# Kernel optimization log

Measured on AMD Instinct MI355X. Metric: run time of the kernel, lower is better.

Reference implementation:

```python
import jax, jax.numpy as jnp
import numpy as np

N = 100000      # nodes
E = 1600000     # edges (avg degree 16)
DIN = 32
DOUT = 32


def setup_inputs() -> dict:
    key = jax.random.key(0)
    k1, k2, k3 = jax.random.split(key, 3)
    x = jax.random.normal(k1, (N, DIN), dtype=jnp.float32)
    edge_index = jax.random.randint(k2, (2, E), 0, N)  # [2, E] (src, dst)
    W = jax.random.normal(k3, (DIN, DOUT), dtype=jnp.float32) / np.sqrt(DIN).astype(np.float32)
    b = jnp.zeros((DOUT,), dtype=jnp.float32)
    return {"x": x, "edge_index": edge_index, "W": W, "b": b}


def reference(x, edge_index, W, b):
    # GCNConv with norm='both' (DGL GraphConv semantics):
    # out = D_dst^{-1/2} * A * (D_src^{-1/2} * X * W) + b
    src, dst = edge_index[0], edge_index[1]
    ones = jnp.ones((edge_index.shape[1],), dtype=x.dtype)
    out_deg = jax.ops.segment_sum(ones, src, num_segments=N)  # out-degree of src nodes
    in_deg = jax.ops.segment_sum(ones, dst, num_segments=N)   # in-degree of dst nodes
    norm_src = jnp.where(out_deg > 0, out_deg ** -0.5, 0.0)   # [N]
    norm_dst = jnp.where(in_deg > 0, in_deg ** -0.5, 0.0)     # [N]
    # feature transform before aggregation (in_feats >= out_feats path)
    h = (x * norm_src[:, None]) @ W                           # [N, DOUT]
    # sparse neighbor aggregation: gather along src, scatter-add to dst
    agg = jax.ops.segment_sum(h[src], dst, num_segments=N)    # [N, DOUT]
    return agg * norm_dst[:, None] + b
```

## Files before the change

### kernel.cpp

```cpp
#include <hip/hip_runtime.h>
#include <hip/hip_bf16.h>

#define DIN 32
#define DOUT 32
#define BINSHIFT 8
#define BINW 256
#define NBMAX 512
#define PTHREADS 512
#define PK 8
#define PB (PTHREADS * PK)
#define SRCBITS 17
#define SRCMASK ((1u << SRCBITS) - 1u)
#define CAP_LDS 8192

__device__ __forceinline__ float bf_lo(unsigned v) { return __uint_as_float(v << 16); }
__device__ __forceinline__ float bf_hi(unsigned v) { return __uint_as_float(v & 0xffff0000u); }
__device__ __forceinline__ unsigned f2bf_rne(float f) {
    unsigned u = __float_as_uint(f);
    return (u + 0x7fffu + ((u >> 16) & 1u)) >> 16;
}

__global__ void init_caps_kernel(int* __restrict__ baseS, int* __restrict__ baseD,
                                 int* __restrict__ curS, int* __restrict__ curD,
                                 int NB, int cap) {
    int i = threadIdx.x;
    if (i <= NB) {
        int v = i * cap;
        baseS[i] = v; baseD[i] = v;
        if (i < NB) { curS[i] = v; curD[i] = v; }
    }
}

__global__ void hist_coarse_kernel(const int* __restrict__ src, const int* __restrict__ dst,
                                   int E, int* __restrict__ gcntS, int* __restrict__ gcntD) {
    __shared__ int hS[NBMAX], hD[NBMAX];
    for (int i = threadIdx.x; i < NBMAX; i += 256) { hS[i] = 0; hD[i] = 0; }
    __syncthreads();
    int stride = gridDim.x * blockDim.x;
    for (int e = blockIdx.x * blockDim.x + threadIdx.x; e < E; e += stride) {
        atomicAdd(&hS[src[e] >> BINSHIFT], 1);
        atomicAdd(&hD[dst[e] >> BINSHIFT], 1);
    }
    __syncthreads();
    for (int i = threadIdx.x; i < NBMAX; i += 256) {
        if (hS[i]) atomicAdd(&gcntS[i], hS[i]);
        if (hD[i]) atomicAdd(&gcntD[i], hD[i]);
    }
}

__global__ void scan_coarse_kernel(const int* __restrict__ gcntS, const int* __restrict__ gcntD,
                                   int* __restrict__ baseS, int* __restrict__ baseD,
                                   int* __restrict__ curS, int* __restrict__ curD,
                                   int NB, int E) {
    __shared__ int s1[NBMAX], s2[NBMAX];
    int t = threadIdx.x;
    int a = (t < NB) ? gcntS[t] : 0;
    int c = (t < NB) ? gcntD[t] : 0;
    s1[t] = a; s2[t] = c;
    for (int o = 1; o < NBMAX; o <<= 1) {
        __syncthreads();
        int x = (t >= o) ? s1[t - o] : 0;
        int y = (t >= o) ? s2[t - o] : 0;
        __syncthreads();
        s1[t] += x; s2[t] += y;
    }
    __syncthreads();
    if (t < NB) {
        baseS[t] = s1[t] - a; curS[t] = s1[t] - a;
        baseD[t] = s2[t] - c; curD[t] = s2[t] - c;
    }
    if (t == 0) { baseS[NB] = E; baseD[NB] = E; }
}

__global__ void partition_both_kernel(const int* __restrict__ src, const int* __restrict__ dst,
                                      int E, int* __restrict__ curS, int* __restrict__ curD,
                                      int* __restrict__ binnedS, int* __restrict__ binnedD) {
    __shared__ int cntS[NBMAX], cntD[NBMAX];
    __shared__ int gbS[NBMAX], gbD[NBMAX];
    __shared__ int stage[PB];
    __shared__ unsigned short sbin[PB];
    int t = threadIdx.x;
    cntS[t] = 0; cntD[t] = 0;
    __syncthreads();

    int base_e = blockIdx.x * PB;
    int nvalid = E - base_e; if (nvalid > PB) nvalid = PB;

    int vs[PK], vd[PK], rkS[PK], rkD[PK];
#pragma unroll
    for (int i = 0; i < PK; ++i) {
        int e = base_e + i * PTHREADS + t;
        if (e < E) {
            int s = src[e], d = dst[e];
            vs[i] = s; vd[i] = d;
            rkS[i] = atomicAdd(&cntS[s >> BINSHIFT], 1);
            rkD[i] = atomicAdd(&cntD[d >> BINSHIFT], 1);
        } else vs[i] = -1;
    }
    __syncthreads();

    int cS = cntS[t], cD = cntD[t];
    for (int o = 1; o < NBMAX; o <<= 1) {
        __syncthreads();
        int xS = (t >= o) ? cntS[t - o] : 0;
        int xD = (t >= o) ? cntD[t - o] : 0;
        __syncthreads();
        cntS[t] += xS; cntD[t] += xD;
    }
    __syncthreads();
    int lS = cntS[t] - cS, lD = cntD[t] - cD;
    int gS = cS ? atomicAdd(&curS[t], cS) : 0;
    int gD = cD ? atomicAdd(&curD[t], cD) : 0;
    gbS[t] = gS - lS; gbD[t] = gD - lD;
    __syncthreads();
    cntS[t] = lS; cntD[t] = lD;
    __syncthreads();

#pragma unroll
    for (int i = 0; i < PK; ++i) {
        if (vs[i] >= 0) {
            int b = vs[i] >> BINSHIFT;
            int slot = cntS[b] + rkS[i];
            stage[slot] = vs[i];
            sbin[slot] = (unsigned short)b;
        }
    }
    __syncthreads();
    for (int i = t; i < nvalid; i += PTHREADS)
        binnedS[gbS[sbin[i]] + i] = stage[i];
    __syncthreads();

#pragma unroll
    for (int i = 0; i < PK; ++i) {
        if (vs[i] >= 0) {
            int b = vd[i] >> BINSHIFT;
            int slot = cntD[b] + rkD[i];
            stage[slot] = ((vd[i] & (BINW - 1)) << SRCBITS) | vs[i];
            sbin[slot] = (unsigned short)b;
        }
    }
    __syncthreads();
    for (int i = t; i < nvalid; i += PTHREADS)
        binnedD[gbD[sbin[i]] + i] = stage[i];
}

__global__ void count_src_kernel(const int* __restrict__ binnedS, const int* __restrict__ baseS,
                                 const int* __restrict__ endS, int* __restrict__ degs, int n) {
    __shared__ int cnt[BINW];
    int b = blockIdx.x;
    int beg = baseS[b], end = endS[b];
    int lo = b << BINSHIFT;
    int t = threadIdx.x;
    cnt[t] = 0;
    __syncthreads();
    for (int e = beg + t; e < end; e += 256) atomicAdd(&cnt[binnedS[e] - lo], 1);
    __syncthreads();
    int node = lo + t;
    if (node < n) degs[node] = cnt[t];
}

__global__ void transform_bf16_kernel(const float* __restrict__ x, const float* __restrict__ W,
                                      const int* __restrict__ degs,
                                      unsigned* __restrict__ h, int n) {
    __shared__ float Ws[32][33];
    __shared__ float xs[16][32];
    int pr = threadIdx.x & 15;
    int r  = threadIdx.x >> 4;

    for (int i = threadIdx.x; i < 32 * 32; i += 256) Ws[i >> 5][i & 31] = W[i];
    int row = blockIdx.x * 16 + r;
    if (row < n) {
        float2 xv = *reinterpret_cast<const float2*>(&x[(size_t)row * 32 + 2 * pr]);
        xs[r][2 * pr] = xv.x; xs[r][2 * pr + 1] = xv.y;
    }
    __syncthreads();

    if (row < n) {
        float a0 = 0.f, a1 = 0.f;
#pragma unroll
        for (int k = 0; k < 32; ++k) {
            float xv = xs[r][k];
            a0 += xv * Ws[k][2 * pr];
            a1 += xv * Ws[k][2 * pr + 1];
        }
        int d = degs[row];
        float nrm = (d > 0) ? rsqrtf((float)d) : 0.f;
        h[(size_t)row * 16 + pr] = f2bf_rne(a0 * nrm) | (f2bf_rne(a1 * nrm) << 16);
    }
}

__global__ void csr_agg_kernel(const int* __restrict__ binnedD, const int* __restrict__ baseD,
                               const int* __restrict__ endD, const uint2* __restrict__ hb,
                               const float* __restrict__ bias, float* __restrict__ out, int n) {
    __shared__ int cnt[BINW];
    __shared__ int start[BINW];
    __shared__ int cur[BINW];
    __shared__ int lesrc[CAP_LDS];

    int t = threadIdx.x;
    int b = blockIdx.x;
    int beg = baseD[b], end = endD[b];
    int lo = b << BINSHIFT;
    int q  = t & 7;
    int ng = t >> 3;

    float4 a0 = {0.f, 0.f, 0.f, 0.f};
    float4 a1 = {0.f, 0.f, 0.f, 0.f};
    int d0 = 0, d1 = 0;

    for (int cb = beg; cb < end; cb += CAP_LDS) {
        int ce = cb + CAP_LDS; if (ce > end) ce = end;
        if (t < BINW) cnt[t] = 0;
        __syncthreads();
        for (int e = cb + t; e < ce; e += 1024)
            atomicAdd(&cnt[((unsigned)binnedD[e]) >> SRCBITS], 1);
        __syncthreads();
        if (t < BINW) start[t] = cnt[t];
        __syncthreads();
        for (int o = 1; o < BINW; o <<= 1) {
            int x = 0;
            if (t < BINW && t >= o) x = start[t - o];
            __syncthreads();
            if (t < BINW) start[t] += x;
            __syncthreads();
        }
        if (t < BINW) { int excl = start[t] - cnt[t]; start[t] = excl; cur[t] = excl; }
        __syncthreads();
        for (int e = cb + t; e < ce; e += 1024) {
            unsigned p = (unsigned)binnedD[e];
            int r = atomicAdd(&cur[p >> SRCBITS], 1);
            lesrc[r] = (int)(p & SRCMASK);
        }
        __syncthreads();
        {
            int kb = start[ng], kc = cnt[ng];
            d0 += kc;
            int k = kb, ke = kb + kc;
            for (; k + 4 <= ke; k += 4) {
                int s0 = lesrc[k], s1 = lesrc[k + 1], s2 = lesrc[k + 2], s3 = lesrc[k + 3];
                uint2 v0 = hb[(size_t)s0 * 8 + q];
                uint2 v1 = hb[(size_t)s1 * 8 + q];
                uint2 v2 = hb[(size_t)s2 * 8 + q];
                uint2 v3 = hb[(size_t)s3 * 8 + q];
                a0.x += bf_lo(v0.x); a0.y += bf_hi(v0.x); a0.z += bf_lo(v0.y); a0.w += bf_hi(v0.y);
                a0.x += bf_lo(v1.x); a0.y += bf_hi(v1.x); a0.z += bf_lo(v1.y); a0.w += bf_hi(v1.y);
                a0.x += bf_lo(v2.x); a0.y += bf_hi(v2.x); a0.z += bf_lo(v2.y); a0.w += bf_hi(v2.y);
                a0.x += bf_lo(v3.x); a0.y += bf_hi(v3.x); a0.z += bf_lo(v3.y); a0.w += bf_hi(v3.y);
            }
            for (; k < ke; ++k) {
                uint2 v = hb[(size_t)lesrc[k] * 8 + q];
                a0.x += bf_lo(v.x); a0.y += bf_hi(v.x); a0.z += bf_lo(v.y); a0.w += bf_hi(v.y);
            }
        }
        {
            int nl = ng + 128;
            int kb = start[nl], kc = cnt[nl];
            d1 += kc;
            int k = kb, ke = kb + kc;
            for (; k + 4 <= ke; k += 4) {
                int s0 = lesrc[k], s1 = lesrc[k + 1], s2 = lesrc[k + 2], s3 = lesrc[k + 3];
                uint2 v0 = hb[(size_t)s0 * 8 + q];
                uint2 v1 = hb[(size_t)s1 * 8 + q];
                uint2 v2 = hb[(size_t)s2 * 8 + q];
                uint2 v3 = hb[(size_t)s3 * 8 + q];
                a1.x += bf_lo(v0.x); a1.y += bf_hi(v0.x); a1.z += bf_lo(v0.y); a1.w += bf_hi(v0.y);
                a1.x += bf_lo(v1.x); a1.y += bf_hi(v1.x); a1.z += bf_lo(v1.y); a1.w += bf_hi(v1.y);
                a1.x += bf_lo(v2.x); a1.y += bf_hi(v2.x); a1.z += bf_lo(v2.y); a1.w += bf_hi(v2.y);
                a1.x += bf_lo(v3.x); a1.y += bf_hi(v3.x); a1.z += bf_lo(v3.y); a1.w += bf_hi(v3.y);
            }
            for (; k < ke; ++k) {
                uint2 v = hb[(size_t)lesrc[k] * 8 + q];
                a1.x += bf_lo(v.x); a1.y += bf_hi(v.x); a1.z += bf_lo(v.y); a1.w += bf_hi(v.y);
            }
        }
        __syncthreads();
    }

    float4 bv = reinterpret_cast<const float4*>(bias)[q];
    int n0 = lo + ng;
    if (n0 < n) {
        float nrm = (d0 > 0) ? rsqrtf((float)d0) : 0.f;
        float4 r;
        r.x = a0.x * nrm + bv.x; r.y = a0.y * nrm + bv.y;
        r.z = a0.z * nrm + bv.z; r.w = a0.w * nrm + bv.w;
        reinterpret_cast<float4*>(&out[(size_t)n0 * 32])[q] = r;
    }
    int n1 = lo + ng + 128;
    if (n1 < n) {
        float nrm = (d1 > 0) ? rsqrtf((float)d1) : 0.f;
        float4 r;
        r.x = a1.x * nrm + bv.x; r.y = a1.y * nrm + bv.y;
        r.z = a1.z * nrm + bv.z; r.w = a1.w * nrm + bv.w;
        reinterpret_cast<float4*>(&out[(size_t)n1 * 32])[q] = r;
    }
}

__global__ void deg_kernel(const int* __restrict__ src, const int* __restrict__ dst,
                           int* __restrict__ degs, int* __restrict__ degd, int E) {
    int i = blockIdx.x * blockDim.x + threadIdx.x;
    if (i < E) {
        atomicAdd(&degs[src[i]], 1);
        atomicAdd(&degd[dst[i]], 1);
    }
}

__global__ void transform_f32_kernel(const float* __restrict__ x, const float* __restrict__ W,
                                     const int* __restrict__ degs, float* __restrict__ h, int n) {
    __shared__ float Ws[32][33];
    __shared__ float xs[8][32];
    int col = threadIdx.x & 31;
    int r   = threadIdx.x >> 5;
    for (int i = threadIdx.x; i < 32 * 32; i += 256) Ws[i >> 5][i & 31] = W[i];
    int row = blockIdx.x * 8 + r;
    xs[r][col] = (row < n) ? x[row * 32 + col] : 0.f;
    __syncthreads();
    if (row < n) {
        float acc = 0.f;
#pragma unroll
        for (int k = 0; k < 32; ++k) acc += xs[r][k] * Ws[k][col];
        int d = degs[row];
        float nrm = (d > 0) ? rsqrtf((float)d) : 0.f;
        h[row * 32 + col] = acc * nrm;
    }
}

__global__ void scatter_kernel(const int* __restrict__ src, const int* __restrict__ dst,
                               const float* __restrict__ h, float* __restrict__ out, int E) {
    int t = blockIdx.x * blockDim.x + threadIdx.x;
    int e = t >> 3;
    int q = t & 7;
    if (e < E) {
        int s = src[e];
        int d = dst[e];
        const float4 v = *reinterpret_cast<const float4*>(&h[s * 32 + q * 4]);
        float* o = &out[d * 32 + q * 4];
        atomicAdd(o + 0, v.x);
        atomicAdd(o + 1, v.y);
        atomicAdd(o + 2, v.z);
        atomicAdd(o + 3, v.w);
    }
}

__global__ void finalize_kernel(float* __restrict__ out, const int* __restrict__ degd,
                                const float* __restrict__ b, int n) {
    int t = blockIdx.x * blockDim.x + threadIdx.x;
    if (t < n * 32) {
        int row = t >> 5;
        int col = t & 31;
        int d = degd[row];
        float nrm = (d > 0) ? rsqrtf((float)d) : 0.f;
        out[t] = out[t] * nrm + b[col];
    }
}

extern "C" void kernel_launch(void* const* d_in, const int* in_sizes, int n_in,
                              void* d_out, int out_size, void* d_ws, size_t ws_size,
                              hipStream_t stream) {
    const float* x  = (const float*)d_in[0];
    const int*   ei = (const int*)d_in[1];
    const float* W  = (const float*)d_in[2];
    const float* bb = (const float*)d_in[3];
    float* out = (float*)d_out;

    const int n = in_sizes[0] / DIN;
    const int E = in_sizes[1] / 2;
    const int* src = ei;
    const int* dst = ei + E;

    const int NB = (n + BINW - 1) >> BINSHIFT;

    int cap = (int)((((long long)E / NB) * 3 / 2 + 255) & ~255LL);
    if (cap < 1024) cap = 1024;

    size_t szH      = ((size_t)n * DOUT * sizeof(__hip_bfloat16) + 15) & ~(size_t)15;
    size_t szBinE   = ((size_t)E * sizeof(int) + 15) & ~(size_t)15;
    size_t szBinCap = ((size_t)NB * cap * sizeof(int) + PB * sizeof(int) + 15) & ~(size_t)15;
    size_t szSmall  = (size_t)n * sizeof(int) + 6 * (NBMAX + 1) * sizeof(int) + 64;

    auto layout = [&](size_t szBin, char* p0, int** binnedS, unsigned** h, int** binnedD,
                      int** degs, int** gcntS, int** gcntD, int** baseS, int** baseD,
                      int** curS, int** curD) -> size_t {
        char* p = p0;
        size_t szR1 = (szBin > szH) ? szBin : szH;
        *binnedS = (int*)p; *h = (unsigned*)p;      p += szR1;
        *binnedD = (int*)p;                         p += szBin;
        *degs    = (int*)p;                         p += (size_t)n * sizeof(int);
        *gcntS   = (int*)p;                         p += NBMAX * sizeof(int);
        *gcntD   = (int*)p;                         p += NBMAX * sizeof(int);
        *baseS   = (int*)p;                         p += (NBMAX + 1) * sizeof(int);
        *baseD   = (int*)p;                         p += (NBMAX + 1) * sizeof(int);
        *curS    = (int*)p;                         p += NBMAX * sizeof(int);
        *curD    = (int*)p;                         p += NBMAX * sizeof(int);
        return (size_t)(p - p0);
    };

    int *binnedS, *binnedD, *degs, *gcntS, *gcntD, *baseS, *baseD, *curS, *curD;
    unsigned* h;

    size_t needed_cap  = szBinCap * 2 + szSmall + ((szBinCap > szH) ? 0 : (szH - szBinCap));

    const int partBlocks = (E + PB - 1) / PB;

    bool ok = (NB <= NBMAX) && (n <= (1 << SRCBITS));

    if (ok) {
        size_t need = layout(szBinCap, (char*)d_ws, &binnedS, &h, &binnedD, &degs,
                             &gcntS, &gcntD, &baseS, &baseD, &curS, &curD);
        if (need <= ws_size) {
            init_caps_kernel<<<1, NBMAX, 0, stream>>>(baseS, baseD, curS, curD, NB, cap);
            partition_both_kernel<<<partBlocks, PTHREADS, 0, stream>>>(src, dst, E, curS, curD,
                                                                       binnedS, binnedD);
            count_src_kernel<<<NB, 256, 0, stream>>>(binnedS, baseS, curS, degs, n);
            transform_bf16_kernel<<<(n + 15) / 16, 256, 0, stream>>>(x, W, degs, h, n);
            csr_agg_kernel<<<NB, 1024, 0, stream>>>(binnedD, baseD, curD, (const uint2*)h,
                                                    bb, out, n);
            return;
        }
        need = layout(szBinE, (char*)d_ws, &binnedS, &h, &binnedD, &degs,
                      &gcntS, &gcntD, &baseS, &baseD, &curS, &curD);
        if (need <= ws_size) {
            hipMemsetAsync(gcntS, 0, 2 * NBMAX * sizeof(int), stream);
            hist_coarse_kernel<<<512, 256, 0, stream>>>(src, dst, E, gcntS, gcntD);
            scan_coarse_kernel<<<1, NBMAX, 0, stream>>>(gcntS, gcntD, baseS, baseD,
                                                        curS, curD, NB, E);
            partition_both_kernel<<<partBlocks, PTHREADS, 0, stream>>>(src, dst, E, curS, curD,
                                                                       binnedS, binnedD);
            count_src_kernel<<<NB, 256, 0, stream>>>(binnedS, baseS, curS, degs, n);
            transform_bf16_kernel<<<(n + 15) / 16, 256, 0, stream>>>(x, W, degs, h, n);
            csr_agg_kernel<<<NB, 1024, 0, stream>>>(binnedD, baseD, curD, (const uint2*)h,
                                                    bb, out, n);
            return;
        }
    }

    {
        float* hf   = (float*)d_ws;
        int*   dgs  = (int*)(hf + (size_t)n * DOUT);
        int*   degd = dgs + n;
        hipMemsetAsync(dgs, 0, (size_t)2 * n * sizeof(int), stream);
        hipMemsetAsync(d_out, 0, (size_t)out_size * sizeof(float), stream);
        deg_kernel<<<(E + 255) / 256, 256, 0, stream>>>(src, dst, dgs, degd, E);
        transform_f32_kernel<<<(n + 7) / 8, 256, 0, stream>>>(x, W, dgs, hf, n);
        long long st = (long long)E * 8;
        scatter_kernel<<<(int)((st + 255) / 256), 256, 0, stream>>>(src, dst, hf, out, E);
        finalize_kernel<<<(n * 32 + 255) / 256, 256, 0, stream>>>(out, degd, bb, n);
    }
}
```

Measured before the change: 79.24 us.

## Fuse source-degree count with feature transform; widen aggregation gathers and single-pass LDS bucketing

```diff
diff --git a/kernel.cpp b/kernel.cpp
--- a/kernel.cpp
+++ b/kernel.cpp
@@ -12,6 +12,7 @@
 #define SRCBITS 17
 #define SRCMASK ((1u << SRCBITS) - 1u)
 #define CAP_LDS 8192
+#define AK (CAP_LDS / 1024)
 
 __device__ __forceinline__ float bf_lo(unsigned v) { return __uint_as_float(v << 16); }
 __device__ __forceinline__ float bf_hi(unsigned v) { return __uint_as_float(v & 0xffff0000u); }
@@ -144,76 +145,79 @@
         binnedD[gbD[sbin[i]] + i] = stage[i];
 }
 
-__global__ void count_src_kernel(const int* __restrict__ binnedS, const int* __restrict__ baseS,
-                                 const int* __restrict__ endS, int* __restrict__ degs, int n) {
-    __shared__ int cnt[BINW];
+__global__ void cnt_transform_kernel(const int* __restrict__ binnedS,
+                                     const int* __restrict__ baseS, const int* __restrict__ endS,
+                                     const float* __restrict__ x, const float* __restrict__ W,
+                                     unsigned* __restrict__ h, int n) {
+    __shared__ int   cnt[BINW];
+    __shared__ float Ws[32][33];
+    __shared__ float xs[32][33];
+    int t = threadIdx.x;
     int b = blockIdx.x;
     int beg = baseS[b], end = endS[b];
     int lo = b << BINSHIFT;
-    int t = threadIdx.x;
-    cnt[t] = 0;
-    __syncthreads();
-    for (int e = beg + t; e < end; e += 256) atomicAdd(&cnt[binnedS[e] - lo], 1);
-    __syncthreads();
-    int node = lo + t;
-    if (node < n) degs[node] = cnt[t];
-}
-
-__global__ void transform_bf16_kernel(const float* __restrict__ x, const float* __restrict__ W,
-                                      const int* __restrict__ degs,
-                                      unsigned* __restrict__ h, int n) {
-    __shared__ float Ws[32][33];
-    __shared__ float xs[16][32];
-    int pr = threadIdx.x & 15;
-    int r  = threadIdx.x >> 4;
-
-    for (int i = threadIdx.x; i < 32 * 32; i += 256) Ws[i >> 5][i & 31] = W[i];
-    int row = blockIdx.x * 16 + r;
-    if (row < n) {
-        float2 xv = *reinterpret_cast<const float2*>(&x[(size_t)row * 32 + 2 * pr]);
-        xs[r][2 * pr] = xv.x; xs[r][2 * pr + 1] = xv.y;
-    }
-    __syncthreads();
-
-    if (row < n) {
-        float a0 = 0.f, a1 = 0.f;
-#pragma unroll
-        for (int k = 0; k < 32; ++k) {
-            float xv = xs[r][k];
-            a0 += xv * Ws[k][2 * pr];
-            a1 += xv * Ws[k][2 * pr + 1];
-        }
-        int d = degs[row];
-        float nrm = (d > 0) ? rsqrtf((float)d) : 0.f;
-        h[(size_t)row * 16 + pr] = f2bf_rne(a0 * nrm) | (f2bf_rne(a1 * nrm) << 16);
+
+    if (t < BINW) cnt[t] = 0;
+    for (int i = t; i < 32 * 32; i += 512) Ws[i >> 5][i & 31] = W[i];
+    __syncthreads();
+    for (int e = beg + t; e < end; e += 512) atomicAdd(&cnt[binnedS[e] - lo], 1);
+    __syncthreads();
+
+    int pr = t & 15, r = t >> 4;
+    for (int pass = 0; pass < 8; ++pass) {
+        int row = lo + pass * 32 + r;
+        if (row < n) {
+            float2 xv = *reinterpret_cast<const float2*>(&x[(size_t)row * 32 + 2 * pr]);
+            xs[r][2 * pr] = xv.x; xs[r][2 * pr + 1] = xv.y;
+        }
+        __syncthreads();
+        if (row < n) {
+            float a0 = 0.f, a1 = 0.f;
+#pragma unroll
+            for (int k = 0; k < 32; ++k) {
+                float xv = xs[r][k];
+                a0 += xv * Ws[k][2 * pr];
+                a1 += xv * Ws[k][2 * pr + 1];
+            }
+            int d = cnt[pass * 32 + r];
+            float nrm = (d > 0) ? rsqrtf((float)d) : 0.f;
+            h[(size_t)row * 16 + pr] = f2bf_rne(a0 * nrm) | (f2bf_rne(a1 * nrm) << 16);
+        }
+        __syncthreads();
     }
 }
 
 __global__ void csr_agg_kernel(const int* __restrict__ binnedD, const int* __restrict__ baseD,
-                               const int* __restrict__ endD, const uint2* __restrict__ hb,
+                               const int* __restrict__ endD, const uint4* __restrict__ hb4,
                                const float* __restrict__ bias, float* __restrict__ out, int n) {
     __shared__ int cnt[BINW];
     __shared__ int start[BINW];
-    __shared__ int cur[BINW];
     __shared__ int lesrc[CAP_LDS];
 
     int t = threadIdx.x;
     int b = blockIdx.x;
     int beg = baseD[b], end = endD[b];
     int lo = b << BINSHIFT;
-    int q  = t & 7;
-    int ng = t >> 3;
-
-    float4 a0 = {0.f, 0.f, 0.f, 0.f};
-    float4 a1 = {0.f, 0.f, 0.f, 0.f};
-    int d0 = 0, d1 = 0;
+    int q  = t & 3;
+    int ng = t >> 2;
+
+    float4 A0 = {0,0,0,0}, A1 = {0,0,0,0};
+    float4 B0 = {0,0,0,0}, B1 = {0,0,0,0};
+    int deg = 0;
 
     for (int cb = beg; cb < end; cb += CAP_LDS) {
         int ce = cb + CAP_LDS; if (ce > end) ce = end;
         if (t < BINW) cnt[t] = 0;
         __syncthreads();
-        for (int e = cb + t; e < ce; e += 1024)
-            atomicAdd(&cnt[((unsigned)binnedD[e]) >> SRCBITS], 1);
+        unsigned pv[AK]; int rk[AK];
+#pragma unroll
+        for (int i = 0; i < AK; ++i) {
+            int e = cb + i * 1024 + t;
+            if (e < ce) {
+                pv[i] = (unsigned)binnedD[e];
+                rk[i] = atomicAdd(&cnt[pv[i] >> SRCBITS], 1);
+            } else pv[i] = 0xFFFFFFFFu;
+        }
         __syncthreads();
         if (t < BINW) start[t] = cnt[t];
         __syncthreads();
@@ -224,74 +228,56 @@
             if (t < BINW) start[t] += x;
             __syncthreads();
         }
-        if (t < BINW) { int excl = start[t] - cnt[t]; start[t] = excl; cur[t] = excl; }
-        __syncthreads();
-        for (int e = cb + t; e < ce; e += 1024) {
-            unsigned p = (unsigned)binnedD[e];
-            int r = atomicAdd(&cur[p >> SRCBITS], 1);
-            lesrc[r] = (int)(p & SRCMASK);
-        }
-        __syncthreads();
-        {
-            int kb = start[ng], kc = cnt[ng];
-            d0 += kc;
-            int k = kb, ke = kb + kc;
-            for (; k + 4 <= ke; k += 4) {
-                int s0 = lesrc[k], s1 = lesrc[k + 1], s2 = lesrc[k + 2], s3 = lesrc[k + 3];
-                uint2 v0 = hb[(size_t)s0 * 8 + q];
-                uint2 v1 = hb[(size_t)s1 * 8 + q];
-                uint2 v2 = hb[(size_t)s2 * 8 + q];
-                uint2 v3 = hb[(size_t)s3 * 8 + q];
-                a0.x += bf_lo(v0.x); a0.y += bf_hi(v0.x); a0.z += bf_lo(v0.y); a0.w += bf_hi(v0.y);
-                a0.x += bf_lo(v1.x); a0.y += bf_hi(v1.x); a0.z += bf_lo(v1.y); a0.w += bf_hi(v1.y);
-                a0.x += bf_lo(v2.x); a0.y += bf_hi(v2.x); a0.z += bf_lo(v2.y); a0.w += bf_hi(v2.y);
-                a0.x += bf_lo(v3.x); a0.y += bf_hi(v3.x); a0.z += bf_lo(v3.y); a0.w += bf_hi(v3.y);
-            }
-            for (; k < ke; ++k) {
-                uint2 v = hb[(size_t)lesrc[k] * 8 + q];
-                a0.x += bf_lo(v.x); a0.y += bf_hi(v.x); a0.z += bf_lo(v.y); a0.w += bf_hi(v.y);
-            }
-        }
-        {
-            int nl = ng + 128;
-            int kb = start[nl], kc = cnt[nl];
-            d1 += kc;
-            int k = kb, ke = kb + kc;
-            for (; k + 4 <= ke; k += 4) {
-                int s0 = lesrc[k], s1 = lesrc[k + 1], s2 = lesrc[k + 2], s3 = lesrc[k + 3];
-                uint2 v0 = hb[(size_t)s0 * 8 + q];
-                uint2 v1 = hb[(size_t)s1 * 8 + q];
-                uint2 v2 = hb[(size_t)s2 * 8 + q];
-                uint2 v3 = hb[(size_t)s3 * 8 + q];
-                a1.x += bf_lo(v0.x); a1.y += bf_hi(v0.x); a1.z += bf_lo(v0.y); a1.w += bf_hi(v0.y);
-                a1.x += bf_lo(v1.x); a1.y += bf_hi(v1.x); a1.z += bf_lo(v1.y); a1.w += bf_hi(v1.y);
-                a1.x += bf_lo(v2.x); a1.y += bf_hi(v2.x); a1.z += bf_lo(v2.y); a1.w += bf_hi(v2.y);
-                a1.x += bf_lo(v3.x); a1.y += bf_hi(v3.x); a1.z += bf_lo(v3.y); a1.w += bf_hi(v3.y);
-            }
-            for (; k < ke; ++k) {
-                uint2 v = hb[(size_t)lesrc[k] * 8 + q];
-                a1.x += bf_lo(v.x); a1.y += bf_hi(v.x); a1.z += bf_lo(v.y); a1.w += bf_hi(v.y);
-            }
-        }
-        __syncthreads();
-    }
-
-    float4 bv = reinterpret_cast<const float4*>(bias)[q];
-    int n0 = lo + ng;
-    if (n0 < n) {
-        float nrm = (d0 > 0) ? rsqrtf((float)d0) : 0.f;
-        float4 r;
-        r.x = a0.x * nrm + bv.x; r.y = a0.y * nrm + bv.y;
-        r.z = a0.z * nrm + bv.z; r.w = a0.w * nrm + bv.w;
-        reinterpret_cast<float4*>(&out[(size_t)n0 * 32])[q] = r;
-    }
-    int n1 = lo + ng + 128;
-    if (n1 < n) {
-        float nrm = (d1 > 0) ? rsqrtf((float)d1) : 0.f;
-        float4 r;
-        r.x = a1.x * nrm + bv.x; r.y = a1.y * nrm + bv.y;
-        r.z = a1.z * nrm + bv.z; r.w = a1.w * nrm + bv.w;
-        reinterpret_cast<float4*>(&out[(size_t)n1 * 32])[q] = r;
+        if (t < BINW) start[t] -= cnt[t];
+        __syncthreads();
+#pragma unroll
+        for (int i = 0; i < AK; ++i)
+            if (pv[i] != 0xFFFFFFFFu)
+                lesrc[start[pv[i] >> SRCBITS] + rk[i]] = (int)(pv[i] & SRCMASK);
+        __syncthreads();
+
+        int kb = start[ng], kc = cnt[ng];
+        deg += kc;
+        int k = kb, ke = kb + kc;
+        for (; k + 4 <= ke; k += 4) {
+            int s0 = lesrc[k], s1 = lesrc[k + 1], s2 = lesrc[k + 2], s3 = lesrc[k + 3];
+            uint4 v0 = hb4[(size_t)s0 * 4 + q];
+            uint4 v1 = hb4[(size_t)s1 * 4 + q];
+            uint4 v2 = hb4[(size_t)s2 * 4 + q];
+            uint4 v3 = hb4[(size_t)s3 * 4 + q];
+            A0.x += bf_lo(v0.x); A0.y += bf_hi(v0.x); A0.z += bf_lo(v0.y); A0.w += bf_hi(v0.y);
+            A1.x += bf_lo(v0.z); A1.y += bf_hi(v0.z); A1.z += bf_lo(v0.w); A1.w += bf_hi(v0.w);
+            B0.x += bf_lo(v1.x); B0.y += bf_hi(v1.x); B0.z += bf_lo(v1.y); B0.w += bf_hi(v1.y);
+            B1.x += bf_lo(v1.z); B1.y += bf_hi(v1.z); B1.z += bf_lo(v1.w); B1.w += bf_hi(v1.w);
+            A0.x += bf_lo(v2.x); A0.y += bf_hi(v2.x); A0.z += bf_lo(v2.y); A0.w += bf_hi(v2.y);
+            A1.x += bf_lo(v2.z); A1.y += bf_hi(v2.z); A1.z += bf_lo(v2.w); A1.w += bf_hi(v2.w);
+            B0.x += bf_lo(v3.x); B0.y += bf_hi(v3.x); B0.z += bf_lo(v3.y); B0.w += bf_hi(v3.y);
+            B1.x += bf_lo(v3.z); B1.y += bf_hi(v3.z); B1.z += bf_lo(v3.w); B1.w += bf_hi(v3.w);
+        }
+        for (; k < ke; ++k) {
+            uint4 v = hb4[(size_t)lesrc[k] * 4 + q];
+            A0.x += bf_lo(v.x); A0.y += bf_hi(v.x); A0.z += bf_lo(v.y); A0.w += bf_hi(v.y);
+            A1.x += bf_lo(v.z); A1.y += bf_hi(v.z); A1.z += bf_lo(v.w); A1.w += bf_hi(v.w);
+        }
+        __syncthreads();
+    }
+
+    A0.x += B0.x; A0.y += B0.y; A0.z += B0.z; A0.w += B0.w;
+    A1.x += B1.x; A1.y += B1.y; A1.z += B1.z; A1.w += B1.w;
+
+    int node = lo + ng;
+    if (node < n) {
+        float nrm = (deg > 0) ? rsqrtf((float)deg) : 0.f;
+        const float4* b4 = reinterpret_cast<const float4*>(bias);
+        float4 bv0 = b4[2 * q], bv1 = b4[2 * q + 1];
+        float4 o0, o1;
+        o0.x = A0.x * nrm + bv0.x; o0.y = A0.y * nrm + bv0.y;
+        o0.z = A0.z * nrm + bv0.z; o0.w = A0.w * nrm + bv0.w;
+        o1.x = A1.x * nrm + bv1.x; o1.y = A1.y * nrm + bv1.y;
+        o1.z = A1.z * nrm + bv1.z; o1.w = A1.w * nrm + bv1.w;
+        float4* o4 = reinterpret_cast<float4*>(out);
+        o4[(size_t)node * 8 + 2 * q]     = o0;
+        o4[(size_t)node * 8 + 2 * q + 1] = o1;
     }
 }
 
@@ -373,50 +359,44 @@
     if (cap < 1024) cap = 1024;
 
     size_t szH      = ((size_t)n * DOUT * sizeof(__hip_bfloat16) + 15) & ~(size_t)15;
-    size_t szBinE   = ((size_t)E * sizeof(int) + 15) & ~(size_t)15;
+    size_t szBinE   = ((size_t)E * sizeof(int) + PB * sizeof(int) + 15) & ~(size_t)15;
     size_t szBinCap = ((size_t)NB * cap * sizeof(int) + PB * sizeof(int) + 15) & ~(size_t)15;
-    size_t szSmall  = (size_t)n * sizeof(int) + 6 * (NBMAX + 1) * sizeof(int) + 64;
-
-    auto layout = [&](size_t szBin, char* p0, int** binnedS, unsigned** h, int** binnedD,
-                      int** degs, int** gcntS, int** gcntD, int** baseS, int** baseD,
+
+    auto layout = [&](size_t szBin, char* p0, int** binnedS, int** binnedD, unsigned** h,
+                      int** gcntS, int** gcntD, int** baseS, int** baseD,
                       int** curS, int** curD) -> size_t {
         char* p = p0;
-        size_t szR1 = (szBin > szH) ? szBin : szH;
-        *binnedS = (int*)p; *h = (unsigned*)p;      p += szR1;
-        *binnedD = (int*)p;                         p += szBin;
-        *degs    = (int*)p;                         p += (size_t)n * sizeof(int);
-        *gcntS   = (int*)p;                         p += NBMAX * sizeof(int);
-        *gcntD   = (int*)p;                         p += NBMAX * sizeof(int);
-        *baseS   = (int*)p;                         p += (NBMAX + 1) * sizeof(int);
-        *baseD   = (int*)p;                         p += (NBMAX + 1) * sizeof(int);
-        *curS    = (int*)p;                         p += NBMAX * sizeof(int);
-        *curD    = (int*)p;                         p += NBMAX * sizeof(int);
+        *binnedS = (int*)p;       p += szBin;
+        *binnedD = (int*)p;       p += szBin;
+        *h       = (unsigned*)p;  p += szH;
+        *gcntS   = (int*)p;       p += NBMAX * sizeof(int);
+        *gcntD   = (int*)p;       p += NBMAX * sizeof(int);
+        *baseS   = (int*)p;       p += (NBMAX + 1) * sizeof(int);
+        *baseD   = (int*)p;       p += (NBMAX + 1) * sizeof(int);
+        *curS    = (int*)p;       p += NBMAX * sizeof(int);
+        *curD    = (int*)p;       p += NBMAX * sizeof(int);
         return (size_t)(p - p0);
     };
 
-    int *binnedS, *binnedD, *degs, *gcntS, *gcntD, *baseS, *baseD, *curS, *curD;
+    int *binnedS, *binnedD, *gcntS, *gcntD, *baseS, *baseD, *curS, *curD;
     unsigned* h;
 
-    size_t needed_cap  = szBinCap * 2 + szSmall + ((szBinCap > szH) ? 0 : (szH - szBinCap));
-
     const int partBlocks = (E + PB - 1) / PB;
-
     bool ok = (NB <= NBMAX) && (n <= (1 << SRCBITS));
 
     if (ok) {
-        size_t need = layout(szBinCap, (char*)d_ws, &binnedS, &h, &binnedD, &degs,
+        size_t need = layout(szBinCap, (char*)d_ws, &binnedS, &binnedD, &h,
                              &gcntS, &gcntD, &baseS, &baseD, &curS, &curD);
         if (need <= ws_size) {
             init_caps_kernel<<<1, NBMAX, 0, stream>>>(baseS, baseD, curS, curD, NB, cap);
             partition_both_kernel<<<partBlocks, PTHREADS, 0, stream>>>(src, dst, E, curS, curD,
                                                                        binnedS, binnedD);
-            count_src_kernel<<<NB, 256, 0, stream>>>(binnedS, baseS, curS, degs, n);
-            transform_bf16_kernel<<<(n + 15) / 16, 256, 0, stream>>>(x, W, degs, h, n);
-            csr_agg_kernel<<<NB, 1024, 0, stream>>>(binnedD, baseD, curD, (const uint2*)h,
+            cnt_transform_kernel<<<NB, 512, 0, stream>>>(binnedS, baseS, curS, x, W, h, n);
+            csr_agg_kernel<<<NB, 1024, 0, stream>>>(binnedD, baseD, curD, (const uint4*)h,
                                                     bb, out, n);
             return;
         }
-        need = layout(szBinE, (char*)d_ws, &binnedS, &h, &binnedD, &degs,
+        need = layout(szBinE, (char*)d_ws, &binnedS, &binnedD, &h,
                       &gcntS, &gcntD, &baseS, &baseD, &curS, &curD);
         if (need <= ws_size) {
             hipMemsetAsync(gcntS, 0, 2 * NBMAX * sizeof(int), stream);
@@ -425,9 +405,8 @@
                                                         curS, curD, NB, E);
             partition_both_kernel<<<partBlocks, PTHREADS, 0, stream>>>(src, dst, E, curS, curD,
                                                                        binnedS, binnedD);
-            count_src_kernel<<<NB, 256, 0, stream>>>(binnedS, baseS, curS, degs, n);
-            transform_bf16_kernel<<<(n + 15) / 16, 256, 0, stream>>>(x, W, degs, h, n);
-            csr_agg_kernel<<<NB, 1024, 0, stream>>>(binnedD, baseD, curD, (const uint2*)h,
+            cnt_transform_kernel<<<NB, 512, 0, stream>>>(binnedS, baseS, curS, x, W, h, n);
+            csr_agg_kernel<<<NB, 1024, 0, stream>>>(binnedD, baseD, curD, (const uint4*)h,
                                                     bb, out, n);
             return;
         }
```

Measured after the change: 81.02 us. 1.02x slower.
